# Kernel optimization log

Measured on AMD Instinct MI355X. Metric: run time of the kernel, lower is better.

## Reference

```python
import jax, jax.numpy as jnp
import numpy as np

P = 1024          # nodes per graph
B = 64            # graphs in batch
N = P * B         # total nodes
E = N * 32        # total edges (avg degree 32)
D_IN = 16         # per-node feature dim (share_obs_dim)
H = 32            # GCN / MLP hidden dim (hardcoded in GNet)
SHARE = 64        # flat share_state dim


def setup_inputs() -> dict:
    key = jax.random.key(0)
    ks = jax.random.split(key, 20)

    x = jax.random.normal(ks[0], (N, D_IN), jnp.float32)
    src = jax.random.randint(ks[1], (E,), 0, N, dtype=jnp.int32)
    # keep edges inside each 1024-node graph block (PyG batched graphs)
    dst = (src // P) * P + jax.random.randint(ks[2], (E,), 0, P, dtype=jnp.int32)
    edge_index = jnp.stack([src, dst])
    value_batch = (jnp.arange(N, dtype=jnp.int32) // P)
    share_state = jax.random.normal(ks[3], (B, SHARE), jnp.float32)

    def lin(k, o, i):
        return jax.random.normal(k, (o, i), jnp.float32) / np.float32(np.sqrt(i))

    return {
        "x": x, "edge_index": edge_index, "value_batch": value_batch,
        "share_state": share_state,
        # value_gnet: GCNConv(D_IN,32), GCNConv(32,32), Linear(32,32), post-pool Linear(32,32)
        "W1": lin(ks[4], H, D_IN), "b1": jnp.zeros((H,), jnp.float32),
        "W2": lin(ks[5], H, H),    "b2": jnp.zeros((H,), jnp.float32),
        "Wl": lin(ks[6], H, H),    "bl": jnp.zeros((H,), jnp.float32),
        "Wp": lin(ks[7], H, H),    "bp": jnp.zeros((H,), jnp.float32),
        # value_net MLP: SHARE->32->32->32
        "Vw1": lin(ks[8], H, SHARE), "Vb1": jnp.zeros((H,), jnp.float32),
        "Vw2": lin(ks[9], H, H),     "Vb2": jnp.zeros((H,), jnp.float32),
        "Vw3": lin(ks[10], H, H),    "Vb3": jnp.zeros((H,), jnp.float32),
        # value_comnet: 64->32->1
        "Cw1": lin(ks[11], H, 2 * H), "Cb1": jnp.zeros((H,), jnp.float32),
        "Cw2": lin(ks[12], 1, H) * np.float32(0.01), "Cb2": jnp.zeros((1,), jnp.float32),
    }


def gcn_conv(x, src, dst, W, b):
    """PyG GCNConv: D^-1/2 (A+I) D^-1/2 X W^T + b (unit edge weights)."""
    n = x.shape[0]
    loop = jnp.arange(n, dtype=src.dtype)
    s = jnp.concatenate([src, loop])
    d = jnp.concatenate([dst, loop])
    deg = jax.ops.segment_sum(jnp.ones(s.shape[0], x.dtype), d, num_segments=n)
    dis = jnp.where(deg > 0, jax.lax.rsqrt(jnp.maximum(deg, 1e-12)), 0.0)
    norm = dis[s] * dis[d]                      # [E+N]
    h = x @ W.T                                  # [N, H] small GEMM first
    out = jax.ops.segment_sum(h[s] * norm[:, None], d, num_segments=n)
    return out + b


def reference(x, edge_index, value_batch, share_state,
              W1, b1, W2, b2, Wl, bl, Wp, bp,
              Vw1, Vb1, Vw2, Vb2, Vw3, Vb3,
              Cw1, Cb1, Cw2, Cb2):
    src, dst = edge_index[0], edge_index[1]
    nb = share_state.shape[0]

    # value_gnet
    h = jnp.tanh(gcn_conv(x, src, dst, W1, b1))
    h = jnp.tanh(gcn_conv(h, src, dst, W2, b2))
    h = jnp.tanh(h @ Wl.T + bl)
    pooled = jax.ops.segment_sum(h, value_batch, num_segments=nb)  # global_add_pool -> [B, 32]
    h1 = pooled @ Wp.T + bp

    # value_net MLP on flat share_state
    h2 = jnp.tanh(share_state @ Vw1.T + Vb1)
    h2 = jnp.tanh(h2 @ Vw2.T + Vb2)
    h2 = h2 @ Vw3.T + Vb3

    # value_comnet
    z = jnp.tanh(jnp.concatenate([h1, h2], axis=-1) @ Cw1.T + Cb1)
    value = z @ Cw2.T + Cb2                      # [B, 1]
    return value
```

## Files before the change

### kernel.cpp

```cpp
#include <hip/hip_runtime.h>
#include <math.h>

#define NNODES 65536
#define NEDGES 2097152
#define PGRAPH 1024
#define NGRAPH 64
#define CAPE_E 34560
#define CAPQ   9728
#define CSRG   (4 * CAPQ)

#define OFF_GFILL 0u
#define OFF_POOL4 256u
#define OFF_ROWI  33024u
#define OFF_DIS   295168u
#define OFF_CSR   557312u
#define OFF_EBUF  5538048u
#define OFF_H1    14385408u

__device__ __forceinline__ float ftanh(float x) {
    float e = __expf(2.f * x);
    return 1.f - 2.f * __builtin_amdgcn_rcpf(e + 1.f);
}

__device__ __forceinline__ unsigned short pack_bf16(float f) {
    unsigned int b = __float_as_uint(f);
    b += 0x7FFFu + ((b >> 16) & 1u);
    return (unsigned short)(b >> 16);
}
__device__ __forceinline__ float unpack_bf16_lo(unsigned int u) {
    return __uint_as_float(u << 16);
}
__device__ __forceinline__ float unpack_bf16_hi(unsigned int u) {
    return __uint_as_float(u & 0xFFFF0000u);
}

__global__ void k_bucket(const int* __restrict__ src, const int* __restrict__ dst,
                         int* __restrict__ gfill, unsigned int* __restrict__ ebuf) {
    __shared__ unsigned int sorted[8192];
    __shared__ int hist[64], lexcl[64], gbase[64], lfill[64];
    int t = threadIdx.x;
    if (t < 64) { hist[t] = 0; lfill[t] = 0; }
    __syncthreads();

    const int4* src4 = (const int4*)(src + blockIdx.x * 8192);
    const int4* dst4 = (const int4*)(dst + blockIdx.x * 8192);
    unsigned int pk[32];
    #pragma unroll
    for (int k = 0; k < 8; k++) {
        int4 s4 = src4[k * 256 + t];
        int4 d4 = dst4[k * 256 + t];
        int ss[4] = { s4.x, s4.y, s4.z, s4.w };
        int dd[4] = { d4.x, d4.y, d4.z, d4.w };
        #pragma unroll
        for (int j = 0; j < 4; j++) {
            int g = ss[j] >> 10;
            pk[k * 4 + j] = (unsigned int)((ss[j] & 1023) | ((dd[j] & 1023) << 10) | (g << 20));
            atomicAdd(&hist[g], 1);
        }
    }
    __syncthreads();
    if (t < 64) {
        int h = hist[t];
        int x = h;
        #pragma unroll
        for (int off = 1; off < 64; off <<= 1) {
            int y = __shfl_up(x, off, 64);
            if (t >= off) x += y;
        }
        lexcl[t] = x - h;
        gbase[t] = atomicAdd(&gfill[t], h);
    }
    __syncthreads();
    #pragma unroll
    for (int k = 0; k < 32; k++) {
        int g = pk[k] >> 20;
        int pos = lexcl[g] + atomicAdd(&lfill[g], 1);
        sorted[pos] = pk[k];
    }
    __syncthreads();
    for (int i = t; i < 8192; i += 256) {
        unsigned int p = sorted[i];
        int g = p >> 20;
        ebuf[(size_t)g * CAPE_E + gbase[g] + (i - lexcl[g])] = p;
    }
}

__global__ __launch_bounds__(1024, 1) void k_build_conv1(
        const float* __restrict__ x, const float* __restrict__ W,
        const float* __restrict__ bias,
        const unsigned int* __restrict__ ebuf, const int* __restrict__ gfill,
        float* __restrict__ disg, unsigned int* __restrict__ rowinfo,
        unsigned short* __restrict__ csr, unsigned short* __restrict__ h1) {
    __shared__ float hsL[1025 * 32];
    __shared__ unsigned short lcsr[CAPQ];
    __shared__ int uhist[1024];
    __shared__ int lrow[256], lfill[256];
    __shared__ int wsum[4];
    float4* hsL4 = (float4*)hsL;

    int t = threadIdx.x;
    int g = blockIdx.x & 63, part = blockIdx.x >> 6;
    int cnt = gfill[g];
    const unsigned int* eb = ebuf + (size_t)g * CAPE_E;

    float inr[16];
    {
        const float4* in4 = (const float4*)(x + ((size_t)(g << 10) + t) * 16);
        #pragma unroll
        for (int k = 0; k < 4; k++) {
            float4 v = in4[k];
            inr[4*k] = v.x; inr[4*k+1] = v.y; inr[4*k+2] = v.z; inr[4*k+3] = v.w;
        }
    }

    uhist[t] = 0;
    if (t < 32) hsL[1024 * 32 + t] = 0.f;
    __syncthreads();
    for (int i = t; i < cnt; i += 1024) atomicAdd(&uhist[(eb[i] >> 10) & 1023], 1);
    __syncthreads();

    int dv_own = uhist[t];
    float dis_own = rsqrtf((float)(dv_own + 1));

    int dq = 0, r4 = 0;
    if (t < 256) { dq = uhist[part * 256 + t]; r4 = (dq + 3) & ~3; }
    int lane = t & 63, wid = t >> 6;
    int xx = r4;
    #pragma unroll
    for (int off = 1; off < 64; off <<= 1) {
        int y = __shfl_up(xx, off, 64);
        if (lane >= off) xx += y;
    }
    if (t < 256 && lane == 63) wsum[wid] = xx;
    __syncthreads();
    if (t < 256) {
        int pre = 0;
        for (int w = 0; w < wid; w++) pre += wsum[w];
        lrow[t] = pre + xx - r4;
        lfill[t] = 0;
    }
    __syncthreads();

    for (int i = t; i < cnt; i += 1024) {
        unsigned int v = eb[i];
        int d = (v >> 10) & 1023;
        if ((d >> 8) == part) {
            int dl = d & 255;
            int pos = lrow[dl] + atomicAdd(&lfill[dl], 1);
            lcsr[pos] = (unsigned short)(v & 1023);
        }
    }
    __syncthreads();
    if (t < 256) {
        int st = lrow[t];
        for (int i = dq; i < r4; i++) lcsr[st + i] = 1024;
        int n = (g << 10) + part * 256 + t;
        disg[n] = rsqrtf((float)(dq + 1));
        rowinfo[n] = ((unsigned int)st << 16) | (unsigned int)dq;
    }
    __syncthreads();

    int qlen = lrow[255] + ((uhist[part * 256 + 255] + 3) & ~3);
    {
        const ushort4* l4 = (const ushort4*)lcsr;
        ushort4* c4 = (ushort4*)(csr + (size_t)g * CSRG + part * CAPQ);
        for (int i = t; i < (qlen >> 2); i += 1024) c4[i] = l4[i];
    }

    {
        int sw = t & 7;
        #pragma unroll
        for (int o4 = 0; o4 < 8; o4++) {
            float r[4];
            #pragma unroll
            for (int j = 0; j < 4; j++) {
                int o = o4 * 4 + j;
                float s = 0.f;
                #pragma unroll
                for (int k = 0; k < 16; k++) s += inr[k] * W[o * 16 + k];
                r[j] = s * dis_own;
            }
            hsL4[t * 8 + (o4 ^ sw)] = make_float4(r[0], r[1], r[2], r[3]);
        }
    }
    __syncthreads();

    int q = t & 7, grp = t >> 3;
    #pragma unroll
    for (int pass = 0; pass < 2; pass++) {
        int lq = pass * 128 + grp;
        int ln = part * 256 + lq;
        int d = uhist[ln];
        float dn = rsqrtf((float)(d + 1));
        int st = lrow[lq];
        float4 acc = hsL4[ln * 8 + (q ^ (ln & 7))];
        const ushort4* c4 = (const ushort4*)(lcsr + st);
        int d4 = (d + 3) >> 2;
        for (int i = 0; i < d4; i++) {
            ushort4 ss = c4[i];
            float4 v0 = hsL4[ss.x * 8 + (q ^ (ss.x & 7))];
            float4 v1 = hsL4[ss.y * 8 + (q ^ (ss.y & 7))];
            float4 v2 = hsL4[ss.z * 8 + (q ^ (ss.z & 7))];
            float4 v3 = hsL4[ss.w * 8 + (q ^ (ss.w & 7))];
            acc.x += (v0.x + v1.x) + (v2.x + v3.x);
            acc.y += (v0.y + v1.y) + (v2.y + v3.y);
            acc.z += (v0.z + v1.z) + (v2.z + v3.z);
            acc.w += (v0.w + v1.w) + (v2.w + v3.w);
        }
        float4 bb = ((const float4*)bias)[q];
        ushort4 r;
        r.x = pack_bf16(ftanh(dn * acc.x + bb.x));
        r.y = pack_bf16(ftanh(dn * acc.y + bb.y));
        r.z = pack_bf16(ftanh(dn * acc.z + bb.z));
        r.w = pack_bf16(ftanh(dn * acc.w + bb.w));
        ((ushort4*)h1)[((size_t)(g << 10) + ln) * 8 + q] = r;
    }
}

__global__ __launch_bounds__(1024, 1) void k_conv2(
        const unsigned short* __restrict__ h1, const float* __restrict__ W,
        const float* __restrict__ bias, const float* __restrict__ disg,
        const unsigned int* __restrict__ rowinfo, const unsigned short* __restrict__ csr,
        const float* __restrict__ Wl, const float* __restrict__ bl,
        float* __restrict__ pooled4) {
    __shared__ float hsL[1025 * 32];
    __shared__ float WlL[32 * 33];
    float4* hsL4 = (float4*)hsL;

    int t = threadIdx.x;
    int g = blockIdx.x & 63, part = blockIdx.x >> 6;

    float inr[32];
    {
        const uint4* in4 = (const uint4*)(h1 + ((size_t)(g << 10) + t) * 32);
        #pragma unroll
        for (int k = 0; k < 4; k++) {
            uint4 v = in4[k];
            unsigned int uu[4] = { v.x, v.y, v.z, v.w };
            #pragma unroll
            for (int j = 0; j < 4; j++) {
                inr[8*k + 2*j]     = unpack_bf16_lo(uu[j]);
                inr[8*k + 2*j + 1] = unpack_bf16_hi(uu[j]);
            }
        }
    }
    float dn_own = disg[(g << 10) + t];

    if (t < 32 * 32) WlL[(t >> 5) * 33 + (t & 31)] = Wl[t];
    if (t < 32) hsL[1024 * 32 + t] = 0.f;
    __syncthreads();

    {
        int sw = t & 7;
        #pragma unroll
        for (int o4 = 0; o4 < 8; o4++) {
            float r[4];
            #pragma unroll
            for (int j = 0; j < 4; j++) {
                int o = o4 * 4 + j;
                float s = 0.f;
                #pragma unroll
                for (int k = 0; k < 32; k++) s += inr[k] * W[o * 32 + k];
                r[j] = s * dn_own;
            }
            hsL4[t * 8 + (o4 ^ sw)] = make_float4(r[0], r[1], r[2], r[3]);
        }
    }
    __syncthreads();

    int q = t & 7, grp = t >> 3;
    float4 racc[2];
    #pragma unroll
    for (int pass = 0; pass < 2; pass++) {
        int lq = pass * 128 + grp;
        int ln = part * 256 + lq;
        int n = (g << 10) + ln;
        unsigned int ri = rowinfo[n];
        int st = ri >> 16;
        int d  = ri & 0xFFFF;
        float dn = rsqrtf((float)(d + 1));
        float4 acc = hsL4[ln * 8 + (q ^ (ln & 7))];
        const ushort4* c4 = (const ushort4*)(csr + (size_t)g * CSRG + part * CAPQ + st);
        int d4 = (d + 3) >> 2;
        for (int i = 0; i < d4; i++) {
            ushort4 ss = c4[i];
            float4 v0 = hsL4[ss.x * 8 + (q ^ (ss.x & 7))];
            float4 v1 = hsL4[ss.y * 8 + (q ^ (ss.y & 7))];
            float4 v2 = hsL4[ss.z * 8 + (q ^ (ss.z & 7))];
            float4 v3 = hsL4[ss.w * 8 + (q ^ (ss.w & 7))];
            acc.x += (v0.x + v1.x) + (v2.x + v3.x);
            acc.y += (v0.y + v1.y) + (v2.y + v3.y);
            acc.z += (v0.z + v1.z) + (v2.z + v3.z);
            acc.w += (v0.w + v1.w) + (v2.w + v3.w);
        }
        float4 bb = ((const float4*)bias)[q];
        float4 r;
        r.x = ftanh(dn * acc.x + bb.x);
        r.y = ftanh(dn * acc.y + bb.y);
        r.z = ftanh(dn * acc.z + bb.z);
        r.w = ftanh(dn * acc.w + bb.w);
        racc[pass] = r;
    }

    __syncthreads();
    #pragma unroll
    for (int pass = 0; pass < 2; pass++) {
        int lnn = pass * 128 + grp;
        hsL4[lnn * 8 + (q ^ (lnn & 7))] = racc[pass];
    }
    __syncthreads();
    int o = t & 31, seg = t >> 5;
    float ps = 0.f;
    #pragma unroll
    for (int j = 0; j < 8; j++) {
        int nl = seg * 8 + j;
        int swn = nl & 7;
        float s = bl[o];
        #pragma unroll
        for (int k = 0; k < 32; k++) {
            float h2v = hsL[nl * 32 + ((((k >> 2) ^ swn) << 2) | (k & 3))];
            s += h2v * WlL[o * 33 + k];
        }
        ps += ftanh(s);
    }
    float* psum = hsL + 8192;
    psum[t] = ps;
    __syncthreads();
    if (t < 32) {
        float tot = 0.f;
        for (int s = 0; s < 32; s++) tot += psum[s * 32 + t];
        pooled4[(g * 4 + part) * 32 + t] = tot;
    }
}

__global__ void k_final(const float* __restrict__ pooled4, const float* __restrict__ share,
                        const float* __restrict__ Wp,  const float* __restrict__ bp,
                        const float* __restrict__ Vw1, const float* __restrict__ Vb1,
                        const float* __restrict__ Vw2, const float* __restrict__ Vb2,
                        const float* __restrict__ Vw3, const float* __restrict__ Vb3,
                        const float* __restrict__ Cw1, const float* __restrict__ Cb1,
                        const float* __restrict__ Cw2, const float* __restrict__ Cb2,
                        float* __restrict__ out) {
    int id = blockIdx.x * 256 + threadIdx.x;
    int b = id >> 5;
    int j = id & 31;
    float p = pooled4[(b * 4 + 0) * 32 + j] + pooled4[(b * 4 + 1) * 32 + j]
            + pooled4[(b * 4 + 2) * 32 + j] + pooled4[(b * 4 + 3) * 32 + j];
    float h1v = bp[j];
    #pragma unroll
    for (int k = 0; k < 32; k++) h1v += Wp[j * 32 + k] * __shfl(p, k, 32);
    float s0 = share[b * 64 + j];
    float s1 = share[b * 64 + 32 + j];
    float t1 = Vb1[j];
    #pragma unroll
    for (int k = 0; k < 32; k++) {
        t1 += Vw1[j * 64 + k] * __shfl(s0, k, 32);
        t1 += Vw1[j * 64 + 32 + k] * __shfl(s1, k, 32);
    }
    t1 = tanhf(t1);
    float t2 = Vb2[j];
    #pragma unroll
    for (int k = 0; k < 32; k++) t2 += Vw2[j * 32 + k] * __shfl(t1, k, 32);
    t2 = tanhf(t2);
    float h2v = Vb3[j];
    #pragma unroll
    for (int k = 0; k < 32; k++) h2v += Vw3[j * 32 + k] * __shfl(t2, k, 32);
    float z = Cb1[j];
    #pragma unroll
    for (int k = 0; k < 32; k++) {
        z += Cw1[j * 64 + k] * __shfl(h1v, k, 32);
        z += Cw1[j * 64 + 32 + k] * __shfl(h2v, k, 32);
    }
    z = tanhf(z);
    float v = Cw2[j] * z;
    v += __shfl_down(v, 16, 32); v += __shfl_down(v, 8, 32);
    v += __shfl_down(v, 4, 32);  v += __shfl_down(v, 2, 32);
    v += __shfl_down(v, 1, 32);
    if (j == 0) out[b] = v + Cb2[0];
}

extern "C" void kernel_launch(void* const* d_in, const int* in_sizes, int n_in,
                              void* d_out, int out_size, void* d_ws, size_t ws_size,
                              hipStream_t stream) {
    const float* x     = (const float*)d_in[0];
    const int*   ei    = (const int*)d_in[1];
    const float* share = (const float*)d_in[3];
    const float* W1 = (const float*)d_in[4];  const float* b1 = (const float*)d_in[5];
    const float* W2 = (const float*)d_in[6];  const float* b2 = (const float*)d_in[7];
    const float* Wl = (const float*)d_in[8];  const float* bl = (const float*)d_in[9];
    const float* Wp = (const float*)d_in[10]; const float* bp = (const float*)d_in[11];
    const float* Vw1 = (const float*)d_in[12]; const float* Vb1 = (const float*)d_in[13];
    const float* Vw2 = (const float*)d_in[14]; const float* Vb2 = (const float*)d_in[15];
    const float* Vw3 = (const float*)d_in[16]; const float* Vb3 = (const float*)d_in[17];
    const float* Cw1 = (const float*)d_in[18]; const float* Cb1 = (const float*)d_in[19];
    const float* Cw2 = (const float*)d_in[20]; const float* Cb2 = (const float*)d_in[21];

    char* ws = (char*)d_ws;
    int*            gfill   = (int*)(ws + OFF_GFILL);
    float*          pooled4 = (float*)(ws + OFF_POOL4);
    unsigned int*   rowinfo = (unsigned int*)(ws + OFF_ROWI);
    float*          disg    = (float*)(ws + OFF_DIS);
    unsigned short* csr     = (unsigned short*)(ws + OFF_CSR);
    unsigned int*   ebuf    = (unsigned int*)(ws + OFF_EBUF);
    unsigned short* h1      = (unsigned short*)(ws + OFF_H1);

    const int* srcp = ei;
    const int* dstp = ei + NEDGES;

    hipMemsetAsync(gfill, 0, 256, stream);

    k_bucket<<<256, 256, 0, stream>>>(srcp, dstp, gfill, ebuf);
    k_build_conv1<<<256, 1024, 0, stream>>>(x, W1, b1, ebuf, gfill,
                                            disg, rowinfo, csr, h1);
    k_conv2<<<256, 1024, 0, stream>>>(h1, W2, b2, disg, rowinfo, csr,
                                      Wl, bl, pooled4);
    k_final<<<8, 256, 0, stream>>>(pooled4, share, Wp, bp, Vw1, Vb1, Vw2, Vb2,
                                   Vw3, Vb3, Cw1, Cb1, Cw2, Cb2, (float*)d_out);
}
```

Baseline: 183.4 us.

## Fuse both GCN layers into one kernel with per-graph inter-block barriers

Edges are now bucketed by graph and destination quarter, so each of the 256 blocks reads only its own edges instead of scanning the whole graph's list. The two conv kernels merge into one: the CSR stays in shared memory across both layers, and the four blocks of a graph synchronise through global atomic counters (after computing degrees and after writing layer-1 output). This removes the global CSR/rowinfo round trip and a kernel launch. In exchange, h1 is stored in fp32 instead of bf16, and the spin-waits assume all 256 blocks are co-resident, which risks deadlock otherwise.

```diff
diff --git a/kernel.cpp b/kernel.cpp
--- a/kernel.cpp
+++ b/kernel.cpp
@@ -5,41 +5,28 @@
 #define NEDGES 2097152
 #define PGRAPH 1024
 #define NGRAPH 64
-#define CAPE_E 34560
+#define CAPB   9216
 #define CAPQ   9728
-#define CSRG   (4 * CAPQ)
 
 #define OFF_GFILL 0u
-#define OFF_POOL4 256u
-#define OFF_ROWI  33024u
-#define OFF_DIS   295168u
-#define OFF_CSR   557312u
-#define OFF_EBUF  5538048u
-#define OFF_H1    14385408u
+#define OFF_ARR   1024u
+#define OFF_POOL4 1536u
+#define OFF_DIS   34304u
+#define OFF_EBUF  296448u
+#define OFF_H1G   9733632u
 
 __device__ __forceinline__ float ftanh(float x) {
     float e = __expf(2.f * x);
     return 1.f - 2.f * __builtin_amdgcn_rcpf(e + 1.f);
 }
 
-__device__ __forceinline__ unsigned short pack_bf16(float f) {
-    unsigned int b = __float_as_uint(f);
-    b += 0x7FFFu + ((b >> 16) & 1u);
-    return (unsigned short)(b >> 16);
-}
-__device__ __forceinline__ float unpack_bf16_lo(unsigned int u) {
-    return __uint_as_float(u << 16);
-}
-__device__ __forceinline__ float unpack_bf16_hi(unsigned int u) {
-    return __uint_as_float(u & 0xFFFF0000u);
-}
-
 __global__ void k_bucket(const int* __restrict__ src, const int* __restrict__ dst,
                          int* __restrict__ gfill, unsigned int* __restrict__ ebuf) {
     __shared__ unsigned int sorted[8192];
-    __shared__ int hist[64], lexcl[64], gbase[64], lfill[64];
+    __shared__ int hist[256], lexcl[256], gbase[256], lfill[256];
+    __shared__ int wsum[4];
     int t = threadIdx.x;
-    if (t < 64) { hist[t] = 0; lfill[t] = 0; }
+    hist[t] = 0; lfill[t] = 0;
     __syncthreads();
 
     const int4* src4 = (const int4*)(src + blockIdx.x * 8192);
@@ -55,53 +42,64 @@
         for (int j = 0; j < 4; j++) {
             int g = ss[j] >> 10;
             pk[k * 4 + j] = (unsigned int)((ss[j] & 1023) | ((dd[j] & 1023) << 10) | (g << 20));
-            atomicAdd(&hist[g], 1);
-        }
-    }
-    __syncthreads();
-    if (t < 64) {
-        int h = hist[t];
-        int x = h;
-        #pragma unroll
-        for (int off = 1; off < 64; off <<= 1) {
-            int y = __shfl_up(x, off, 64);
-            if (t >= off) x += y;
-        }
-        lexcl[t] = x - h;
+            int b = (g << 2) | ((dd[j] >> 8) & 3);
+            atomicAdd(&hist[b], 1);
+        }
+    }
+    __syncthreads();
+
+    int h = hist[t];
+    int lane = t & 63, wid = t >> 6;
+    int xx = h;
+    #pragma unroll
+    for (int off = 1; off < 64; off <<= 1) {
+        int y = __shfl_up(xx, off, 64);
+        if (lane >= off) xx += y;
+    }
+    if (lane == 63) wsum[wid] = xx;
+    __syncthreads();
+    {
+        int pre = 0;
+        for (int w = 0; w < wid; w++) pre += wsum[w];
+        lexcl[t] = pre + xx - h;
         gbase[t] = atomicAdd(&gfill[t], h);
     }
     __syncthreads();
+
     #pragma unroll
     for (int k = 0; k < 32; k++) {
-        int g = pk[k] >> 20;
-        int pos = lexcl[g] + atomicAdd(&lfill[g], 1);
+        int b = pk[k] >> 18;
+        int pos = lexcl[b] + atomicAdd(&lfill[b], 1);
         sorted[pos] = pk[k];
     }
     __syncthreads();
     for (int i = t; i < 8192; i += 256) {
         unsigned int p = sorted[i];
-        int g = p >> 20;
-        ebuf[(size_t)g * CAPE_E + gbase[g] + (i - lexcl[g])] = p;
-    }
-}
-
-__global__ __launch_bounds__(1024, 1) void k_build_conv1(
-        const float* __restrict__ x, const float* __restrict__ W,
-        const float* __restrict__ bias,
+        int b = p >> 18;
+        ebuf[(size_t)b * CAPB + gbase[b] + (i - lexcl[b])] = p;
+    }
+}
+
+__global__ __launch_bounds__(1024, 1) void k_gcn(
+        const float* __restrict__ x,
+        const float* __restrict__ W1, const float* __restrict__ b1,
+        const float* __restrict__ W2, const float* __restrict__ b2,
+        const float* __restrict__ Wl, const float* __restrict__ bl,
         const unsigned int* __restrict__ ebuf, const int* __restrict__ gfill,
-        float* __restrict__ disg, unsigned int* __restrict__ rowinfo,
-        unsigned short* __restrict__ csr, unsigned short* __restrict__ h1) {
+        float* __restrict__ disg, float* __restrict__ h1g,
+        int* __restrict__ arrive, float* __restrict__ pooled4) {
     __shared__ float hsL[1025 * 32];
     __shared__ unsigned short lcsr[CAPQ];
-    __shared__ int uhist[1024];
-    __shared__ int lrow[256], lfill[256];
+    __shared__ float WlL[32 * 33];
+    __shared__ int hist[256], lrow[256], lfill[256];
     __shared__ int wsum[4];
     float4* hsL4 = (float4*)hsL;
 
     int t = threadIdx.x;
     int g = blockIdx.x & 63, part = blockIdx.x >> 6;
-    int cnt = gfill[g];
-    const unsigned int* eb = ebuf + (size_t)g * CAPE_E;
+    int bkt = (g << 2) | part;
+    int cnt = gfill[bkt];
+    const unsigned int* eb = ebuf + (size_t)bkt * CAPB;
 
     float inr[16];
     {
@@ -113,17 +111,23 @@
         }
     }
 
-    uhist[t] = 0;
+    if (t < 256) hist[t] = 0;
+    WlL[(t >> 5) * 33 + (t & 31)] = Wl[t];
     if (t < 32) hsL[1024 * 32 + t] = 0.f;
     __syncthreads();
-    for (int i = t; i < cnt; i += 1024) atomicAdd(&uhist[(eb[i] >> 10) & 1023], 1);
-    __syncthreads();
-
-    int dv_own = uhist[t];
-    float dis_own = rsqrtf((float)(dv_own + 1));
+
+    for (int i = t; i < cnt; i += 1024) atomicAdd(&hist[(eb[i] >> 10) & 255], 1);
+    __syncthreads();
 
     int dq = 0, r4 = 0;
-    if (t < 256) { dq = uhist[part * 256 + t]; r4 = (dq + 3) & ~3; }
+    if (t < 256) {
+        dq = hist[t]; r4 = (dq + 3) & ~3;
+        disg[(g << 10) + part * 256 + t] = rsqrtf((float)(dq + 1));
+    }
+    __syncthreads();
+    if (t == 0)
+        __hip_atomic_fetch_add(arrive + g, 1, __ATOMIC_RELEASE, __HIP_MEMORY_SCOPE_AGENT);
+
     int lane = t & 63, wid = t >> 6;
     int xx = r4;
     #pragma unroll
@@ -143,45 +147,36 @@
 
     for (int i = t; i < cnt; i += 1024) {
         unsigned int v = eb[i];
-        int d = (v >> 10) & 1023;
-        if ((d >> 8) == part) {
-            int dl = d & 255;
-            int pos = lrow[dl] + atomicAdd(&lfill[dl], 1);
-            lcsr[pos] = (unsigned short)(v & 1023);
-        }
-    }
-    __syncthreads();
+        int dl = (v >> 10) & 255;
+        int pos = lrow[dl] + atomicAdd(&lfill[dl], 1);
+        lcsr[pos] = (unsigned short)(v & 1023);
+    }
     if (t < 256) {
         int st = lrow[t];
         for (int i = dq; i < r4; i++) lcsr[st + i] = 1024;
-        int n = (g << 10) + part * 256 + t;
-        disg[n] = rsqrtf((float)(dq + 1));
-        rowinfo[n] = ((unsigned int)st << 16) | (unsigned int)dq;
-    }
-    __syncthreads();
-
-    int qlen = lrow[255] + ((uhist[part * 256 + 255] + 3) & ~3);
-    {
-        const ushort4* l4 = (const ushort4*)lcsr;
-        ushort4* c4 = (ushort4*)(csr + (size_t)g * CSRG + part * CAPQ);
-        for (int i = t; i < (qlen >> 2); i += 1024) c4[i] = l4[i];
-    }
-
-    {
-        int sw = t & 7;
-        #pragma unroll
-        for (int o4 = 0; o4 < 8; o4++) {
-            float r[4];
+    }
+
+    if (t == 0) {
+        while (__hip_atomic_load(arrive + g, __ATOMIC_RELAXED, __HIP_MEMORY_SCOPE_AGENT) < 4) {}
+        (void)__hip_atomic_load(arrive + g, __ATOMIC_ACQUIRE, __HIP_MEMORY_SCOPE_AGENT);
+    }
+    __syncthreads();
+
+    float dis_t = disg[(g << 10) + t];
+    int sw = t & 7;
+
+    #pragma unroll
+    for (int o4 = 0; o4 < 8; o4++) {
+        float r[4];
+        #pragma unroll
+        for (int j = 0; j < 4; j++) {
+            int o = o4 * 4 + j;
+            float s = 0.f;
             #pragma unroll
-            for (int j = 0; j < 4; j++) {
-                int o = o4 * 4 + j;
-                float s = 0.f;
-                #pragma unroll
-                for (int k = 0; k < 16; k++) s += inr[k] * W[o * 16 + k];
-                r[j] = s * dis_own;
-            }
-            hsL4[t * 8 + (o4 ^ sw)] = make_float4(r[0], r[1], r[2], r[3]);
-        }
+            for (int k = 0; k < 16; k++) s += inr[k] * W1[o * 16 + k];
+            r[j] = s * dis_t;
+        }
+        hsL4[t * 8 + (o4 ^ sw)] = make_float4(r[0], r[1], r[2], r[3]);
     }
     __syncthreads();
 
@@ -190,7 +185,7 @@
     for (int pass = 0; pass < 2; pass++) {
         int lq = pass * 128 + grp;
         int ln = part * 256 + lq;
-        int d = uhist[ln];
+        int d = hist[lq];
         float dn = rsqrtf((float)(d + 1));
         int st = lrow[lq];
         float4 acc = hsL4[ln * 8 + (q ^ (ln & 7))];
@@ -207,80 +202,56 @@
             acc.z += (v0.z + v1.z) + (v2.z + v3.z);
             acc.w += (v0.w + v1.w) + (v2.w + v3.w);
         }
-        float4 bb = ((const float4*)bias)[q];
-        ushort4 r;
-        r.x = pack_bf16(ftanh(dn * acc.x + bb.x));
-        r.y = pack_bf16(ftanh(dn * acc.y + bb.y));
-        r.z = pack_bf16(ftanh(dn * acc.z + bb.z));
-        r.w = pack_bf16(ftanh(dn * acc.w + bb.w));
-        ((ushort4*)h1)[((size_t)(g << 10) + ln) * 8 + q] = r;
-    }
-}
-
-__global__ __launch_bounds__(1024, 1) void k_conv2(
-        const unsigned short* __restrict__ h1, const float* __restrict__ W,
-        const float* __restrict__ bias, const float* __restrict__ disg,
-        const unsigned int* __restrict__ rowinfo, const unsigned short* __restrict__ csr,
-        const float* __restrict__ Wl, const float* __restrict__ bl,
-        float* __restrict__ pooled4) {
-    __shared__ float hsL[1025 * 32];
-    __shared__ float WlL[32 * 33];
-    float4* hsL4 = (float4*)hsL;
-
-    int t = threadIdx.x;
-    int g = blockIdx.x & 63, part = blockIdx.x >> 6;
-
-    float inr[32];
+        float4 bb = ((const float4*)b1)[q];
+        float4 r;
+        r.x = ftanh(dn * acc.x + bb.x);
+        r.y = ftanh(dn * acc.y + bb.y);
+        r.z = ftanh(dn * acc.z + bb.z);
+        r.w = ftanh(dn * acc.w + bb.w);
+        ((float4*)h1g)[((size_t)(g << 10) + ln) * 8 + q] = r;
+    }
+    __syncthreads();
+    if (t == 0) {
+        __hip_atomic_fetch_add(arrive + 64 + g, 1, __ATOMIC_RELEASE, __HIP_MEMORY_SCOPE_AGENT);
+        while (__hip_atomic_load(arrive + 64 + g, __ATOMIC_RELAXED, __HIP_MEMORY_SCOPE_AGENT) < 4) {}
+        (void)__hip_atomic_load(arrive + 64 + g, __ATOMIC_ACQUIRE, __HIP_MEMORY_SCOPE_AGENT);
+    }
+    __syncthreads();
+
+    float r2[32];
     {
-        const uint4* in4 = (const uint4*)(h1 + ((size_t)(g << 10) + t) * 32);
-        #pragma unroll
-        for (int k = 0; k < 4; k++) {
-            uint4 v = in4[k];
-            unsigned int uu[4] = { v.x, v.y, v.z, v.w };
+        const float4* h4 = (const float4*)(h1g + ((size_t)(g << 10) + t) * 32);
+        #pragma unroll
+        for (int k = 0; k < 8; k++) {
+            float4 v = h4[k];
+            r2[4*k] = v.x; r2[4*k+1] = v.y; r2[4*k+2] = v.z; r2[4*k+3] = v.w;
+        }
+    }
+    #pragma unroll
+    for (int o4 = 0; o4 < 8; o4++) {
+        float r[4];
+        #pragma unroll
+        for (int j = 0; j < 4; j++) {
+            int o = o4 * 4 + j;
+            float s = 0.f;
             #pragma unroll
-            for (int j = 0; j < 4; j++) {
-                inr[8*k + 2*j]     = unpack_bf16_lo(uu[j]);
-                inr[8*k + 2*j + 1] = unpack_bf16_hi(uu[j]);
-            }
-        }
-    }
-    float dn_own = disg[(g << 10) + t];
-
-    if (t < 32 * 32) WlL[(t >> 5) * 33 + (t & 31)] = Wl[t];
-    if (t < 32) hsL[1024 * 32 + t] = 0.f;
-    __syncthreads();
-
-    {
-        int sw = t & 7;
-        #pragma unroll
-        for (int o4 = 0; o4 < 8; o4++) {
-            float r[4];
-            #pragma unroll
-            for (int j = 0; j < 4; j++) {
-                int o = o4 * 4 + j;
-                float s = 0.f;
-                #pragma unroll
-                for (int k = 0; k < 32; k++) s += inr[k] * W[o * 32 + k];
-                r[j] = s * dn_own;
-            }
-            hsL4[t * 8 + (o4 ^ sw)] = make_float4(r[0], r[1], r[2], r[3]);
-        }
-    }
-    __syncthreads();
-
-    int q = t & 7, grp = t >> 3;
+            for (int k = 0; k < 32; k++) s += r2[k] * W2[o * 32 + k];
+            r[j] = s * dis_t;
+        }
+        hsL4[t * 8 + (o4 ^ sw)] = make_float4(r[0], r[1], r[2], r[3]);
+    }
+    __syncthreads();
+
     float4 racc[2];
     #pragma unroll
     for (int pass = 0; pass < 2; pass++) {
         int lq = pass * 128 + grp;
         int ln = part * 256 + lq;
-        int n = (g << 10) + ln;
-        unsigned int ri = rowinfo[n];
-        int st = ri >> 16;
-        int d  = ri & 0xFFFF;
+        int d = hist[lq];
         float dn = rsqrtf((float)(d + 1));
+        int st = lrow[lq];
         float4 acc = hsL4[ln * 8 + (q ^ (ln & 7))];
-        const ushort4* c4 = (const ushort4*)(csr + (size_t)g * CSRG + part * CAPQ + st);
+        const ushort4* c4 = (const ushort4*)(lcsr + st);
         int d4 = (d + 3) >> 2;
         for (int i = 0; i < d4; i++) {
             ushort4 ss = c4[i];
@@ -293,7 +264,7 @@
             acc.z += (v0.z + v1.z) + (v2.z + v3.z);
             acc.w += (v0.w + v1.w) + (v2.w + v3.w);
         }
-        float4 bb = ((const float4*)bias)[q];
+        float4 bb = ((const float4*)b2)[q];
         float4 r;
         r.x = ftanh(dn * acc.x + bb.x);
         r.y = ftanh(dn * acc.y + bb.y);
@@ -396,24 +367,21 @@
     const float* Cw2 = (const float*)d_in[20]; const float* Cb2 = (const float*)d_in[21];
 
     char* ws = (char*)d_ws;
-    int*            gfill   = (int*)(ws + OFF_GFILL);
-    float*          pooled4 = (float*)(ws + OFF_POOL4);
-    unsigned int*   rowinfo = (unsigned int*)(ws + OFF_ROWI);
-    float*          disg    = (float*)(ws + OFF_DIS);
-    unsigned short* csr     = (unsigned short*)(ws + OFF_CSR);
-    unsigned int*   ebuf    = (unsigned int*)(ws + OFF_EBUF);
-    unsigned short* h1      = (unsigned short*)(ws + OFF_H1);
+    int*          gfill   = (int*)(ws + OFF_GFILL);
+    int*          arrive  = (int*)(ws + OFF_ARR);
+    float*        pooled4 = (float*)(ws + OFF_POOL4);
+    float*        disg    = (float*)(ws + OFF_DIS);
+    unsigned int* ebuf    = (unsigned int*)(ws + OFF_EBUF);
+    float*        h1g     = (float*)(ws + OFF_H1G);
 
     const int* srcp = ei;
     const int* dstp = ei + NEDGES;
 
-    hipMemsetAsync(gfill, 0, 256, stream);
+    hipMemsetAsync(ws, 0, 1536, stream);
 
     k_bucket<<<256, 256, 0, stream>>>(srcp, dstp, gfill, ebuf);
-    k_build_conv1<<<256, 1024, 0, stream>>>(x, W1, b1, ebuf, gfill,
-                                            disg, rowinfo, csr, h1);
-    k_conv2<<<256, 1024, 0, stream>>>(h1, W2, b2, disg, rowinfo, csr,
-                                      Wl, bl, pooled4);
+    k_gcn<<<256, 1024, 0, stream>>>(x, W1, b1, W2, b2, Wl, bl,
+                                    ebuf, gfill, disg, h1g, arrive, pooled4);
     k_final<<<8, 256, 0, stream>>>(pooled4, share, Wp, bp, Vw1, Vb1, Vw2, Vb2,
                                    Vw3, Vb3, Cw1, Cb1, Cw2, Cb2, (float*)d_out);
 }
```

Result: faster. 179.2 us (-2.3%).
